# Kernel optimization log

Hardware: AMD Instinct MI355X
Metric: run time of the kernel (lower is better)

## Reference

```python
import jax, jax.numpy as jnp
import numpy as np

N = 4096      # nodes
E = 131072    # edges (avg degree 32)
C = 256       # in/hidden channels
NC = 10       # classes
RATIO = 0.5
DEPTH = 2


def _build_adj(edge_index, w, n):
    # COO -> dense, duplicate edges summed (matches CSR coalescing)
    A = jnp.zeros((n, n), jnp.float32)
    return A.at[edge_index[0], edge_index[1]].add(w)


def _gcn(x, A, W, b, fill=2.0):
    # gcn_norm with improved=True: add_remaining_self_loops(fill=2.0),
    # deg from target (col) sums, sym norm; out[i] = sum_j Anorm[j,i] * (xW)[j]
    n = A.shape[0]
    idx = jnp.arange(n)
    diag = A[idx, idx]
    A = A.at[idx, idx].set(jnp.where(diag != 0, diag, fill))
    deg = A.sum(axis=0)
    dinv = jnp.where(deg > 0, jax.lax.rsqrt(deg), 0.0)
    An = dinv[:, None] * A * dinv[None, :]
    return An.T @ (x @ W) + b


def _augment(A):
    # remove_self_loops + add_self_loops(weight 1) == set diag to 1,
    # then adj @ adj, then remove self loops again
    n = A.shape[0]
    idx = jnp.arange(n)
    A = A.at[idx, idx].set(1.0)
    A2 = A @ A
    return A2.at[idx, idx].set(0.0)


def _pool(x, A, p, k):
    # TopKPooling: score = tanh(x.p / ||p||), keep top-k nodes, gate x by score
    score = jnp.tanh((x @ p) / jnp.linalg.norm(p))
    vals, perm = jax.lax.top_k(score, k)
    x2 = x[perm] * vals[:, None]
    A2 = A[perm][:, perm]   # filter_adj: keep edges with both ends selected
    return x2, A2


def reference(x, edge_index, w0, b0, w1, b1, w2, b2, p1, p2, wc, bc):
    A = _build_adj(edge_index, jnp.ones((edge_index.shape[1],), x.dtype), x.shape[0])
    x = jax.nn.relu(_gcn(x, A, w0, b0))
    k = x.shape[0]
    for (W, b, p) in ((w1, b1, p1), (w2, b2, p2)):
        A = _augment(A)
        k = int(np.ceil(RATIO * k))  # static per level (single graph)
        x, A = _pool(x, A, p, k)
        x = jax.nn.relu(_gcn(x, A, W, b))
    emb = x.mean(axis=0, keepdims=True)                      # global_mean_pool, batch all-zero
    emb = emb / jnp.maximum(jnp.linalg.norm(emb, axis=-1, keepdims=True), 1e-12)
    logits = emb @ wc.T + bc
    return emb, jax.nn.log_softmax(logits, axis=1)


def setup_inputs() -> dict:
    key = jax.random.key(0)
    ks = jax.random.split(key, 12)
    s = 1.0 / np.sqrt(C)
    return {
        'x': jax.random.normal(ks[0], (N, C), jnp.float32),
        'edge_index': jax.random.randint(ks[1], (2, E), 0, N, jnp.int64) if jax.config.jax_enable_x64 else jax.random.randint(ks[1], (2, E), 0, N, jnp.int32),
        'w0': jax.random.normal(ks[2], (C, C), jnp.float32) * s,
        'b0': jnp.zeros((C,), jnp.float32),
        'w1': jax.random.normal(ks[3], (C, C), jnp.float32) * s,
        'b1': jnp.zeros((C,), jnp.float32),
        'w2': jax.random.normal(ks[4], (C, C), jnp.float32) * s,
        'b2': jnp.zeros((C,), jnp.float32),
        'p1': jax.random.normal(ks[5], (C,), jnp.float32) * s,
        'p2': jax.random.normal(ks[6], (C,), jnp.float32) * s,
        'wc': jax.random.normal(ks[7], (NC, C), jnp.float32) * s,
        'bc': jnp.zeros((NC,), jnp.float32),
    }
```

## Files before the change

kernel.cpp:

```cpp
#include <hip/hip_runtime.h>
#include <math.h>

#define CH 256

typedef short short8 __attribute__((ext_vector_type(8)));
typedef float f32x4 __attribute__((ext_vector_type(4)));

__device__ inline ushort f2bf(float f) {
  unsigned u = __float_as_uint(f);
  unsigned r = (u + 0x7FFFu + ((u >> 16) & 1u)) >> 16;
  return (ushort)r;
}

__device__ inline void gload16(const void* g, void* l) {
  __builtin_amdgcn_global_load_lds((const __attribute__((address_space(1))) void*)g,
                                   (__attribute__((address_space(3))) void*)l, 16, 0, 0);
}


__global__ void scatter_edges(const int* __restrict__ ei, int E, int n, float* __restrict__ A) {
  int e = blockIdx.x * blockDim.x + threadIdx.x;
  if (e < E) atomicAdd(&A[(size_t)ei[e] * n + ei[E + e]], 1.0f);
}

template <int DIAGMODE>
__global__ __launch_bounds__(256) void transpose_deg(const float* __restrict__ In, int n,
                                                     ushort* __restrict__ O, float* __restrict__ deg,
                                                     int zn, size_t zoff) {
  __shared__ float t[64][65];
  int j0 = blockIdx.x * 64, i0 = blockIdx.y * 64;
  int tx = threadIdx.x & 63, ty4 = threadIdx.x >> 6;
  float s = 0.f;
#pragma unroll
  for (int r = 0; r < 64; r += 4) {
    int gi = i0 + ty4 + r, gj = j0 + tx;
    size_t idx = (size_t)gi * n + gj;
    float v = In[idx];
    for (int z = 1; z < zn; ++z) v += In[idx + (size_t)z * zoff];
    if (gi == gj) v = (DIAGMODE == 1) ? 2.0f : ((v != 0.f) ? v : 2.0f);
    t[ty4 + r][tx] = v;
    s += v;
  }
  atomicAdd(&deg[j0 + tx], s);
  __syncthreads();
#pragma unroll
  for (int r = 0; r < 64; r += 4) {
    int c = ty4 + r;
    O[(size_t)(j0 + c) * n + i0 + tx] = f2bf(t[tx][c]);
  }
}

__global__ __launch_bounds__(1024) void topk_sort(const float* __restrict__ sc, int n, int k,
                                                  int* __restrict__ perm, float* __restrict__ vals) {
  __shared__ unsigned long long key[4096];
  int tid = threadIdx.x;
  for (int i = tid; i < n; i += 1024) {
    unsigned u = __float_as_uint(sc[i]);
    u = (u & 0x80000000u) ? ~u : (u | 0x80000000u);
    key[i] = ((unsigned long long)u << 32) | (0xFFFFFFFFu - (unsigned)i);
  }
  __syncthreads();
  for (int size = 2; size <= n; size <<= 1) {
    for (int stride = size >> 1; stride > 0; stride >>= 1) {
      for (int i = tid; i < n; i += 1024) {
        int j = i ^ stride;
        if (j > i) {
          unsigned long long ka = key[i], kb = key[j];
          bool up = ((i & size) == 0);
          bool pj = kb > ka;
          if (up ? pj : !pj) { key[i] = kb; key[j] = ka; }
        }
      }
      __syncthreads();
    }
  }
  for (int i = tid; i < k; i += 1024) {
    unsigned long long kk = key[i];
    unsigned u = (unsigned)(kk >> 32);
    u = (u & 0x80000000u) ? (u & 0x7FFFFFFFu) : ~u;
    perm[i] = (int)(0xFFFFFFFFu - (unsigned)(kk & 0xFFFFFFFFu));
    vals[i] = __uint_as_float(u);
  }
}

__global__ void pool_x(const float* __restrict__ x, const int* __restrict__ perm,
                       const float* __restrict__ vals, float* __restrict__ xo) {
  int i = blockIdx.x, c = threadIdx.x;
  xo[(size_t)i * CH + c] = x[(size_t)perm[i] * CH + c] * vals[i];
}


__global__ void rowgather_cvt(const float* __restrict__ A, const int* __restrict__ perm,
                              int n, ushort* __restrict__ O) {
  int m = blockIdx.y;
  int src = perm[m];
  int k4 = (blockIdx.x * 256 + threadIdx.x) * 4;
  float4 v = *(const float4*)&A[(size_t)src * n + k4];
  if (src >= k4 && src < k4 + 4) ((float*)&v)[src - k4] = 1.0f;
  ushort4 o;
  o.x = f2bf(v.x); o.y = f2bf(v.y); o.z = f2bf(v.z); o.w = f2bf(v.w);
  *(ushort4*)&O[(size_t)m * n + k4] = o;
}

__global__ void rowgather_bf16(const ushort* __restrict__ At, const int* __restrict__ perm,
                               int n, ushort* __restrict__ O) {
  int m = blockIdx.y;
  int src = perm[m];
  int k8 = (blockIdx.x * 256 + threadIdx.x) * 8;
  uint4 v = *(const uint4*)&At[(size_t)src * n + k8];
  if (src >= k8 && src < k8 + 8) ((ushort*)&v)[src - k8] = 0x3F80;
  *(uint4*)&O[(size_t)m * n + k8] = v;
}


__device__ inline void stage_tile(const ushort* ag, const ushort* bg, int ktOff,
                                  char* asb, char* bsb, int K) {
#pragma unroll
  for (int i = 0; i < 4; ++i)
    gload16(ag + (size_t)i * 32 * K + ktOff, asb + i * 4096);
#pragma unroll
  for (int i = 0; i < 2; ++i)
    gload16(bg + (size_t)i * 32 * K + ktOff, bsb + i * 4096);
}

__device__ inline void compute_tile(const ushort (*__restrict__ As)[64],
                                    const ushort (*__restrict__ Bs)[64],
                                    int wm, int wn, int lrow, int col0, int col1,
                                    f32x4 acc[4][2]) {
#pragma unroll
  for (int ks = 0; ks < 2; ++ks) {
    const int col = ks ? col1 : col0;
    short8 af[4], bf[2];
#pragma unroll
    for (int t = 0; t < 4; ++t)
      af[t] = *(const short8*)&As[wm + t * 16 + lrow][col];
#pragma unroll
    for (int t = 0; t < 2; ++t)
      bf[t] = *(const short8*)&Bs[wn + t * 16 + lrow][col];
#pragma unroll
    for (int mt = 0; mt < 4; ++mt)
#pragma unroll
      for (int nt = 0; nt < 2; ++nt)
        acc[mt][nt] = __builtin_amdgcn_mfma_f32_16x16x32_bf16(af[mt], bf[nt], acc[mt][nt], 0, 0, 0);
  }
}

__global__ __launch_bounds__(256) void mfma_nt(const ushort* __restrict__ Aop,
                                               const ushort* __restrict__ Bop,
                                               float* __restrict__ C, int ldc,
                                               int K, int Ks, size_t zstride) {
  __shared__ ushort As[3][128][64];
  __shared__ ushort Bs[3][64][64];
  const int tid = threadIdx.x;
  const int wave = tid >> 6, lane = tid & 63;
  const int wm = (wave & 1) * 64, wn = (wave >> 1) * 32;
  const int m0 = blockIdx.x * 128, n0 = blockIdx.y * 64;
  const int k0 = blockIdx.z * Ks;
  C += (size_t)blockIdx.z * zstride;
  const int lrow = lane & 15;
  const int q = lane >> 4;
  const int rx = lane & 7;
  const int col0 = ((q)     ^ rx) * 8;
  const int col1 = ((4 + q) ^ rx) * 8;
  const int srow = wave * 8 + (lane >> 3);
  const int scol = ((lane & 7) ^ (lane >> 3)) * 8;
  const ushort* ag = Aop + (size_t)(m0 + srow) * K + k0 + scol;
  const ushort* bg = Bop + (size_t)(n0 + srow) * K + k0 + scol;
  f32x4 acc[4][2] = {};

  const int nk = Ks >> 6;

#define STAGE(bi, idx) stage_tile(ag, bg, (idx) * 64, \
    (char*)&As[bi][0][0] + wave * 1024, (char*)&Bs[bi][0][0] + wave * 1024, K)

  STAGE(0, 0);
  if (1 < nk) STAGE(1, 1);
  if (2 < nk) STAGE(2, 2);

  int bi = 0;
  for (int t = 0; t < nk - 2; ++t) {
    asm volatile("s_waitcnt vmcnt(12)" ::: "memory");
    __builtin_amdgcn_s_barrier();
    __builtin_amdgcn_sched_barrier(0);
    compute_tile(As[bi], Bs[bi], wm, wn, lrow, col0, col1, acc);
    __builtin_amdgcn_sched_barrier(0);
    __builtin_amdgcn_s_barrier();
    if (t + 3 < nk) STAGE(bi, t + 3);
    bi = (bi + 1 < 3) ? bi + 1 : 0;
  }
  asm volatile("s_waitcnt vmcnt(6)" ::: "memory");
  __builtin_amdgcn_s_barrier();
  __builtin_amdgcn_sched_barrier(0);
  compute_tile(As[bi], Bs[bi], wm, wn, lrow, col0, col1, acc);
  bi = (bi + 1 < 3) ? bi + 1 : 0;
  asm volatile("s_waitcnt vmcnt(0)" ::: "memory");
  __builtin_amdgcn_s_barrier();
  __builtin_amdgcn_sched_barrier(0);
  compute_tile(As[bi], Bs[bi], wm, wn, lrow, col0, col1, acc);
#undef STAGE

  const int crow = (lane >> 4) * 4, ccol = lane & 15;
#pragma unroll
  for (int mt = 0; mt < 4; ++mt)
#pragma unroll
    for (int nt = 0; nt < 2; ++nt) {
      int gm = m0 + wm + mt * 16 + crow;
      int gn = n0 + wn + nt * 16 + ccol;
#pragma unroll
      for (int r = 0; r < 4; ++r)
        C[(size_t)(gm + r) * ldc + gn] = acc[mt][nt][r];
    }
}

__global__ void agg_epilogue(const float* __restrict__ Cred, size_t zstride, int zn,
                             const float* __restrict__ deg,
                             const float* __restrict__ bias, float* __restrict__ xo,
                             const float* __restrict__ p, float* __restrict__ sc) {
  int idx = blockIdx.x * 256 + threadIdx.x;
  int c4 = idx & 63;
  int m = idx >> 6;
  float d = deg[m];
  float s = (d > 0.f) ? 1.0f / sqrtf(d) : 0.f;
  float4 v = ((const float4*)Cred)[idx];
  for (int z = 1; z < zn; ++z) {
    float4 u = ((const float4*)(Cred + (size_t)z * zstride))[idx];
    v.x += u.x; v.y += u.y; v.z += u.z; v.w += u.w;
  }
  float4 b = ((const float4*)bias)[c4];
  v.x = fmaxf(fmaf(v.x, s, b.x), 0.f);
  v.y = fmaxf(fmaf(v.y, s, b.y), 0.f);
  v.z = fmaxf(fmaf(v.z, s, b.z), 0.f);
  v.w = fmaxf(fmaf(v.w, s, b.w), 0.f);
  ((float4*)xo)[idx] = v;
  if (p) {
    float4 pv = ((const float4*)p)[c4];
    float dot = v.x * pv.x + v.y * pv.y + v.z * pv.z + v.w * pv.w;
    float pn  = pv.x * pv.x + pv.y * pv.y + pv.z * pv.z + pv.w * pv.w;
    for (int off = 32; off; off >>= 1) {
      dot += __shfl_down(dot, off);
      pn  += __shfl_down(pn, off);
    }
    if ((threadIdx.x & 63) == 0) sc[m] = tanhf(dot / sqrtf(pn));
  }
}

__global__ __launch_bounds__(256) void xw_gemm(const float* __restrict__ Am,
                                               const float* __restrict__ Bm,
                                               ushort* __restrict__ Gt,
                                               int M, const float* __restrict__ deg) {
  __shared__ float As[16][64];
  __shared__ float Bs[16][64];
  const int tid = threadIdx.x;
  const int m0 = blockIdx.x * 64, n0 = blockIdx.y * 64;
  float acc[4][4] = {{0.f}};
  const int tm = tid & 15, tn = tid >> 4;

  for (int kt = 0; kt < CH; kt += 16) {
    __syncthreads();
    {
      int mm = tid >> 2, kq = (tid & 3) * 4;
      float4 v = *(const float4*)(Am + (size_t)(m0 + mm) * CH + kt + kq);
      As[kq + 0][mm] = v.x; As[kq + 1][mm] = v.y; As[kq + 2][mm] = v.z; As[kq + 3][mm] = v.w;
    }
#pragma unroll
    for (int r = 0; r < 4; ++r) {
      int idx = tid + r * 256;
      int kk = idx >> 6, nn = idx & 63;
      Bs[kk][nn] = Bm[(size_t)(kt + kk) * CH + (n0 + nn)];
    }
    __syncthreads();
#pragma unroll
    for (int kk = 0; kk < 16; ++kk) {
      float4 a = *(const float4*)&As[kk][tm * 4];
      float4 b = *(const float4*)&Bs[kk][tn * 4];
      acc[0][0] = fmaf(a.x, b.x, acc[0][0]);
      acc[0][1] = fmaf(a.x, b.y, acc[0][1]);
      acc[0][2] = fmaf(a.x, b.z, acc[0][2]);
      acc[0][3] = fmaf(a.x, b.w, acc[0][3]);
      acc[1][0] = fmaf(a.y, b.x, acc[1][0]);
      acc[1][1] = fmaf(a.y, b.y, acc[1][1]);
      acc[1][2] = fmaf(a.y, b.z, acc[1][2]);
      acc[1][3] = fmaf(a.y, b.w, acc[1][3]);
      acc[2][0] = fmaf(a.z, b.x, acc[2][0]);
      acc[2][1] = fmaf(a.z, b.y, acc[2][1]);
      acc[2][2] = fmaf(a.z, b.z, acc[2][2]);
      acc[2][3] = fmaf(a.z, b.w, acc[2][3]);
      acc[3][0] = fmaf(a.w, b.x, acc[3][0]);
      acc[3][1] = fmaf(a.w, b.y, acc[3][1]);
      acc[3][2] = fmaf(a.w, b.z, acc[3][2]);
      acc[3][3] = fmaf(a.w, b.w, acc[3][3]);
    }
  }

#pragma unroll
  for (int ii = 0; ii < 4; ++ii) {
    int m = m0 + tm * 4 + ii;
    float d = deg[m];
    float s = (d > 0.f) ? 1.0f / sqrtf(d) : 0.f;
#pragma unroll
    for (int jj = 0; jj < 4; ++jj) {
      int n = n0 + tn * 4 + jj;
      Gt[(size_t)n * M + m] = f2bf(s * acc[ii][jj]);
    }
  }
}


__global__ void mean_partial(const float* __restrict__ x2, float* __restrict__ macc) {
  int c = threadIdx.x;
  int j0 = blockIdx.x * 16;
  float s = 0.f;
#pragma unroll
  for (int j = 0; j < 16; ++j) s += x2[(size_t)(j0 + j) * CH + c];
  atomicAdd(&macc[c], s);
}

__global__ __launch_bounds__(256) void finalize2(const float* __restrict__ macc, int nr,
                                                 const float* __restrict__ wc,
                                                 const float* __restrict__ bc,
                                                 float* __restrict__ out) {
  __shared__ float semb[256];
  __shared__ float red[256];
  __shared__ float slog[16];
  int c = threadIdx.x;
  float emb = macc[c] / (float)nr;
  red[c] = emb * emb;
  __syncthreads();
  for (int off = 128; off; off >>= 1) {
    if (c < off) red[c] += red[c + off];
    __syncthreads();
  }
  float denom = fmaxf(sqrtf(red[0]), 1e-12f);
  float en = emb / denom;
  semb[c] = en;
  out[c] = en;
  __syncthreads();
  if (c < 10) {
    float l = bc[c];
    for (int t = 0; t < CH; ++t) l = fmaf(semb[t], wc[c * CH + t], l);
    slog[c] = l;
  }
  __syncthreads();
  if (c == 0) {
    float mx = slog[0];
    for (int j = 1; j < 10; ++j) mx = fmaxf(mx, slog[j]);
    float se = 0.f;
    for (int j = 0; j < 10; ++j) se += expf(slog[j] - mx);
    float lse = mx + logf(se);
    for (int j = 0; j < 10; ++j) out[CH + j] = slog[j] - lse;
  }
}


extern "C" void kernel_launch(void* const* d_in, const int* in_sizes, int n_in,
                              void* d_out, int out_size, void* d_ws, size_t ws_size,
                              hipStream_t stream) {
  const float* x  = (const float*)d_in[0];
  const int*   ei = (const int*)d_in[1];
  const float* w0 = (const float*)d_in[2];
  const float* b0 = (const float*)d_in[3];
  const float* w1 = (const float*)d_in[4];
  const float* b1 = (const float*)d_in[5];
  const float* w2 = (const float*)d_in[6];
  const float* b2 = (const float*)d_in[7];
  const float* p1 = (const float*)d_in[8];
  const float* p2 = (const float*)d_in[9];
  const float* wc = (const float*)d_in[10];
  const float* bc = (const float*)d_in[11];
  float* out = (float*)d_out;
  const int N0 = 4096, K1 = 2048, K2 = 1024;
  int E = in_sizes[1] / 2;

  float* W = (float*)d_ws;
  size_t off = 0;
  float* A    = W + off; off += (size_t)N0 * N0;
  float* Pa   = W + off; off += (size_t)K1 * K1;
  ushort* At  = (ushort*)(W + off); off += (size_t)N0 * N0 / 2;
  ushort* Arow = (ushort*)(W + off); off += (size_t)K1 * N0 / 2;
  ushort* Brow = (ushort*)A;
  float* Paux = A + (size_t)8 * 1024 * 1024;
  float* Cred = (float*)Arow;
  float* x0   = W + off; off += (size_t)N0 * CH;
  ushort* Gt  = (ushort*)(W + off); off += (size_t)N0 * CH / 2;
  float* xp  = W + off; off += (size_t)K1 * CH;
  float* x1  = W + off; off += (size_t)K1 * CH;
  float* x2  = W + off; off += (size_t)K2 * CH;
  float* sc  = W + off; off += 4096;
  float* vals = W + off; off += 4096;
  float* deg  = W + off; off += 4096;
  float* macc = W + off; off += 256;
  int* perm1 = (int*)(W + off); off += 4096;
  int* perm2 = (int*)(W + off); off += 4096;

  hipMemsetAsync(A, 0, (size_t)N0 * N0 * 4, stream);
  scatter_edges<<<(E + 255) / 256, 256, 0, stream>>>(ei, E, N0, A);

  hipMemsetAsync(deg, 0, N0 * 4, stream);
  transpose_deg<0><<<dim3(N0 / 64, N0 / 64), 256, 0, stream>>>(A, N0, At, deg, 1, 0);
  xw_gemm<<<dim3(N0 / 64, CH / 64), 256, 0, stream>>>(x, w0, Gt, N0, deg);
  mfma_nt<<<dim3(N0 / 128, CH / 64, 4), 256, 0, stream>>>(At, Gt, Cred, CH, N0, N0 / 4, (size_t)N0 * CH);
  agg_epilogue<<<N0 / 4, 256, 0, stream>>>(Cred, (size_t)N0 * CH, 4, deg, b0, x0, p1, sc);

  topk_sort<<<1, 1024, 0, stream>>>(sc, N0, K1, perm1, vals);

  rowgather_cvt<<<dim3(N0 / 1024, K1), 256, 0, stream>>>(A, perm1, N0, Arow);
  rowgather_bf16<<<dim3(N0 / 2048, K1), 256, 0, stream>>>(At, perm1, N0, Brow);
  mfma_nt<<<dim3(K1 / 128, K1 / 64, 1), 256, 0, stream>>>(Arow, Brow, Pa, K1, N0, N0, 0);
  pool_x<<<K1, 256, 0, stream>>>(x0, perm1, vals, xp);

  hipMemsetAsync(deg, 0, K1 * 4, stream);
  transpose_deg<1><<<dim3(K1 / 64, K1 / 64), 256, 0, stream>>>(Pa, K1, At, deg, 1, 0);
  xw_gemm<<<dim3(K1 / 64, CH / 64), 256, 0, stream>>>(xp, w1, Gt, K1, deg);
  mfma_nt<<<dim3(K1 / 128, CH / 64, 8), 256, 0, stream>>>(At, Gt, Cred, CH, K1, K1 / 8, (size_t)K1 * CH);
  agg_epilogue<<<K1 / 4, 256, 0, stream>>>(Cred, (size_t)K1 * CH, 8, deg, b1, x1, p2, sc);

  topk_sort<<<1, 1024, 0, stream>>>(sc, K1, K2, perm2, vals);

  rowgather_cvt<<<dim3(K1 / 1024, K2), 256, 0, stream>>>(Pa, perm2, K1, Arow);
  rowgather_bf16<<<dim3(K1 / 2048, K2), 256, 0, stream>>>(At, perm2, K1, Brow);
  mfma_nt<<<dim3(K2 / 128, K2 / 64, 4), 256, 0, stream>>>(Arow, Brow, Paux, K2, K1, K1 / 4, (size_t)K2 * K2);
  pool_x<<<K2, 256, 0, stream>>>(x1, perm2, vals, xp);

  hipMemsetAsync(deg, 0, K2 * 4, stream);
  transpose_deg<1><<<dim3(K2 / 64, K2 / 64), 256, 0, stream>>>(Paux, K2, At, deg, 4, (size_t)K2 * K2);
  xw_gemm<<<dim3(K2 / 64, CH / 64), 256, 0, stream>>>(xp, w2, Gt, K2, deg);
  mfma_nt<<<dim3(K2 / 128, CH / 64, 4), 256, 0, stream>>>(At, Gt, Cred, CH, K2, K2 / 4, (size_t)K2 * CH);
  agg_epilogue<<<K2 / 4, 256, 0, stream>>>(Cred, (size_t)K2 * CH, 4, deg, b2, x2, nullptr, nullptr);

  hipMemsetAsync(macc, 0, 256 * 4, stream);
  mean_partial<<<K2 / 16, 256, 0, stream>>>(x2, macc);
  finalize2<<<1, 256, 0, stream>>>(macc, K2, wc, bc, out);
}
```

Before: 469.1 us.

## Replace single-block bitonic top-k sort with multi-block rank counting

Swaps the one-block bitonic sort of all scores for a rank-based selection. Each element counts how many unique keys are greater than its own, and that count is its output position, with the work spread over n/64 blocks of 256 threads. This removes the serial barrier-heavy sort that runs on one CU, at the cost of O(n^2) comparisons and every block reloading all keys into LDS.

```diff
diff --git a/kernel.cpp b/kernel.cpp
--- a/kernel.cpp
+++ b/kernel.cpp
@@ -50,36 +50,33 @@
   }
 }
 
-__global__ __launch_bounds__(1024) void topk_sort(const float* __restrict__ sc, int n, int k,
-                                                  int* __restrict__ perm, float* __restrict__ vals) {
-  __shared__ unsigned long long key[4096];
+__global__ __launch_bounds__(256) void topk_rank(const float* __restrict__ sc, int n, int k,
+                                                 int* __restrict__ perm, float* __restrict__ vals) {
+  extern __shared__ unsigned long long kbuf[];
+  __shared__ int red[4][64];
   int tid = threadIdx.x;
-  for (int i = tid; i < n; i += 1024) {
+  for (int i = tid; i < n; i += 256) {
     unsigned u = __float_as_uint(sc[i]);
     u = (u & 0x80000000u) ? ~u : (u | 0x80000000u);
-    key[i] = ((unsigned long long)u << 32) | (0xFFFFFFFFu - (unsigned)i);
-  }
-  __syncthreads();
-  for (int size = 2; size <= n; size <<= 1) {
-    for (int stride = size >> 1; stride > 0; stride >>= 1) {
-      for (int i = tid; i < n; i += 1024) {
-        int j = i ^ stride;
-        if (j > i) {
-          unsigned long long ka = key[i], kb = key[j];
-          bool up = ((i & size) == 0);
-          bool pj = kb > ka;
-          if (up ? pj : !pj) { key[i] = kb; key[j] = ka; }
-        }
-      }
-      __syncthreads();
-    }
-  }
-  for (int i = tid; i < k; i += 1024) {
-    unsigned long long kk = key[i];
-    unsigned u = (unsigned)(kk >> 32);
-    u = (u & 0x80000000u) ? (u & 0x7FFFFFFFu) : ~u;
-    perm[i] = (int)(0xFFFFFFFFu - (unsigned)(kk & 0xFFFFFFFFu));
-    vals[i] = __uint_as_float(u);
+    kbuf[i] = ((unsigned long long)u << 32) | (0xFFFFFFFFu - (unsigned)i);
+  }
+  __syncthreads();
+  const int ti = tid & 63, tj = tid >> 6;
+  const int i = blockIdx.x * 64 + ti;
+  const unsigned long long ki = kbuf[i];
+  int cnt = 0;
+  const int q = n >> 2;
+  const int jb = tj * q, je = jb + q;
+#pragma unroll 4
+  for (int j = jb; j < je; j += 2) {
+    unsigned long long k0 = kbuf[j], k1 = kbuf[j + 1];
+    cnt += (k0 > ki) + (k1 > ki);
+  }
+  red[tj][ti] = cnt;
+  __syncthreads();
+  if (tid < 64) {
+    int r = red[0][ti] + red[1][ti] + red[2][ti] + red[3][ti];
+    if (r < k) { perm[r] = i; vals[r] = sc[i]; }
   }
 }
 
@@ -401,7 +398,7 @@
   mfma_nt<<<dim3(N0 / 128, CH / 64, 4), 256, 0, stream>>>(At, Gt, Cred, CH, N0, N0 / 4, (size_t)N0 * CH);
   agg_epilogue<<<N0 / 4, 256, 0, stream>>>(Cred, (size_t)N0 * CH, 4, deg, b0, x0, p1, sc);
 
-  topk_sort<<<1, 1024, 0, stream>>>(sc, N0, K1, perm1, vals);
+  topk_rank<<<N0 / 64, 256, N0 * 8, stream>>>(sc, N0, K1, perm1, vals);
 
   rowgather_cvt<<<dim3(N0 / 1024, K1), 256, 0, stream>>>(A, perm1, N0, Arow);
   rowgather_bf16<<<dim3(N0 / 2048, K1), 256, 0, stream>>>(At, perm1, N0, Brow);
@@ -414,7 +411,7 @@
   mfma_nt<<<dim3(K1 / 128, CH / 64, 8), 256, 0, stream>>>(At, Gt, Cred, CH, K1, K1 / 8, (size_t)K1 * CH);
   agg_epilogue<<<K1 / 4, 256, 0, stream>>>(Cred, (size_t)K1 * CH, 8, deg, b1, x1, p2, sc);
 
-  topk_sort<<<1, 1024, 0, stream>>>(sc, K1, K2, perm2, vals);
+  topk_rank<<<K1 / 64, 256, K1 * 8, stream>>>(sc, K1, K2, perm2, vals);
 
   rowgather_cvt<<<dim3(K1 / 1024, K2), 256, 0, stream>>>(Pa, perm2, K1, Arow);
   rowgather_bf16<<<dim3(K1 / 2048, K2), 256, 0, stream>>>(At, perm2, K1, Brow);
```

Result: faster. 414.9 us (-11.5%).
